# Performance work log

Measured on AMD Instinct MI355X. Metric: run time of the kernel, lower is better.

Reference implementation:

```python
import jax, jax.numpy as jnp
import numpy as np

GRID_SIZE = 5
SPLINE_ORDER = 3
NUM_EXPERTS = 8
TOP_K = 2
CAP_FACTOR = 1.25
TEMP = 1.0
GDHW = (4, 4, 4)


def make_grid(in_features):
    # efficient-KAN grid buffer: grid_range=[-1,1], extended by spline_order on each side
    h = 2.0 / GRID_SIZE
    g = jnp.arange(-SPLINE_ORDER, GRID_SIZE + SPLINE_ORDER + 1, dtype=jnp.float32) * h - 1.0
    return jnp.broadcast_to(g, (in_features, g.shape[0]))


def b_splines(x, grid):
    # x: (N, in) -> (N, in, GRID_SIZE + SPLINE_ORDER) Cox-de Boor bases
    x = x[:, :, None]
    bases = ((x >= grid[:, :-1]) & (x < grid[:, 1:])).astype(x.dtype)
    for k in range(1, SPLINE_ORDER + 1):
        left = (x - grid[:, : -(k + 1)]) / (grid[:, k:-1] - grid[:, : -(k + 1)])
        right = (grid[:, k + 1:] - x) / (grid[:, k + 1:] - grid[:, 1:-k])
        bases = left * bases[:, :, :-1] + right * bases[:, :, 1:]
    return bases


def kan_linear(x, base_w, spline_w, scaler, grid):
    base = jax.nn.silu(x) @ base_w.T
    bs = b_splines(x, grid)                                   # (N, in, coef)
    spline = jnp.einsum('nic,oic->no', bs, spline_w * scaler[:, :, None])
    return base + spline


def layernorm(x, w, b, eps=1e-5):
    mu = x.mean(-1, keepdims=True)
    var = x.var(-1, keepdims=True)
    return (x - mu) / jnp.sqrt(var + eps) * w + b


def setup_inputs() -> dict:
    key = jax.random.key(0)
    ks = jax.random.split(key, 12)
    Cf, hidden, E, nc = 256, 170, NUM_EXPERTS, 2
    coef = GRID_SIZE + SPLINE_ORDER
    def nrm(k, shape, scale):
        return jax.random.normal(k, shape, dtype=jnp.float32) * scale
    return {
        'fpn_feat': nrm(ks[0], (8, 254, 32, 32, 32), 1.0),
        'seg_logits': nrm(ks[1], (8, 2, 32, 32, 32), 1.0),
        'ln_r_w': jnp.ones((Cf,), jnp.float32),
        'ln_r_b': jnp.zeros((Cf,), jnp.float32),
        'ln_h_w': jnp.ones((Cf,), jnp.float32),
        'ln_h_b': jnp.zeros((Cf,), jnp.float32),
        'router_w': nrm(ks[2], (E, Cf), Cf ** -0.5),
        'router_b': jnp.zeros((E,), jnp.float32),
        'bw1': nrm(ks[3], (E, hidden, Cf), Cf ** -0.5),
        'sw1': nrm(ks[4], (E, hidden, Cf, coef), 0.1 * Cf ** -0.5),
        'sc1': nrm(ks[5], (E, hidden, Cf), Cf ** -0.5),
        'bw2': nrm(ks[6], (E, Cf, hidden), hidden ** -0.5),
        'sw2': nrm(ks[7], (E, Cf, hidden, coef), 0.1 * hidden ** -0.5),
        'sc2': nrm(ks[8], (E, Cf, hidden), hidden ** -0.5),
        'cls_bw': nrm(ks[9], (nc, Cf), Cf ** -0.5),
        'cls_sw': nrm(ks[10], (nc, Cf, coef), 0.1 * Cf ** -0.5),
        'cls_sc': nrm(ks[11], (nc, Cf), Cf ** -0.5),
        'grid_cf': make_grid(Cf),
        'grid_hid': make_grid(hidden),
    }


def reference(fpn_feat, seg_logits, ln_r_w, ln_r_b, ln_h_w, ln_h_b,
              router_w, router_b, bw1, sw1, sc1, bw2, sw2, sc2,
              cls_bw, cls_sw, cls_sc, grid_cf, grid_hid):
    fused = jnp.concatenate([fpn_feat, seg_logits], axis=1)   # (B, Cf, D, H, W)
    B, C, D, H, W = fused.shape
    gd, gh, gw = GDHW
    dp, hp, wp = D // gd, H // gh, W // gw
    # split into gd*gh*gw blocks per sample
    blk = fused.reshape(B, C, gd, dp, gh, hp, gw, wp)
    blk = blk.transpose(0, 2, 4, 6, 1, 3, 5, 7).reshape(-1, C, dp, hp, wp)
    vec = blk.mean(axis=(2, 3, 4))                            # (N, Cf) global avg pool

    N = vec.shape[0]
    E = NUM_EXPERTS
    x_norm = layernorm(vec, ln_r_w, ln_r_b)
    scores = (x_norm @ router_w.T + router_b) / TEMP          # (N, E)
    top_val, top_idx = jax.lax.top_k(scores, TOP_K)
    top_w = jax.nn.softmax(top_val, axis=-1)
    capacity = int(CAP_FACTOR * N * TOP_K / E) + 1

    onehot = top_idx[None] == jnp.arange(E)[:, None, None]    # (E, N, K)
    sel = onehot.any(-1)                                      # (E, N)
    pos = jnp.cumsum(sel.astype(jnp.int32), axis=1)           # rank among selected (1-based)
    keep = sel & (pos <= capacity)                            # capacity drop = first-come order
    w = (top_w[None] * onehot.astype(top_w.dtype)).sum(-1)    # (E, N) combine weights

    def expert(bw1e, sw1e, sc1e, bw2e, sw2e, sc2e):
        h = kan_linear(x_norm, bw1e, sw1e, sc1e, grid_cf)
        h = jax.nn.gelu(h, approximate=False)                 # torch nn.GELU default (erf)
        return kan_linear(h, bw2e, sw2e, sc2e, grid_hid)

    y_all = jax.vmap(expert)(bw1, sw1, sc1, bw2, sw2, sc2)    # (E, N, Cf)
    out = jnp.einsum('en,enc->nc', keep.astype(vec.dtype) * w, y_all)

    conf = scores.max(-1)                                     # (N,)
    logits_blk = kan_linear(layernorm(out, ln_h_w, ln_h_b), cls_bw, cls_sw, cls_sc, grid_cf)
    P = gd * gh * gw
    weight = jax.nn.softmax(conf.reshape(B, P), axis=-1)[:, :, None]
    logits = (logits_blk.reshape(B, P, -1) * weight).sum(1)   # (B, num_classes)
    return logits
```

## Files before the change

kernel.cpp:

```cpp
#include <hip/hip_runtime.h>
#include <math.h>

#define CF 256
#define HID 170
#define NE 8
#define NTOK 512
#define K1 2304
#define K2P 1536
#define CAPACITY 161

typedef __bf16 bf16x8 __attribute__((ext_vector_type(8)));
typedef unsigned short u16x8 __attribute__((ext_vector_type(8)));
typedef float f32x4 __attribute__((ext_vector_type(4)));

__device__ __forceinline__ float silu_f(float x) { return x / (1.0f + expf(-x)); }
__device__ __forceinline__ float gelu_f(float x) {
    return 0.5f * x * (1.0f + erff(x * 0.70710678118654752f));
}

__device__ __forceinline__ unsigned short f2bf(float f) {
    unsigned int u = __float_as_uint(f);
    u = u + 0x7fffu + ((u >> 16) & 1u);
    return (unsigned short)(u >> 16);
}

__device__ __forceinline__ void bspline8(float x, float bs[8]) {
    float b[11];
#pragma unroll
    for (int j = 0; j < 11; ++j) {
        float g0 = (float)(j - 3) * 0.4f - 1.0f;
        float g1 = (float)(j - 2) * 0.4f - 1.0f;
        b[j] = (x >= g0 && x < g1) ? 1.0f : 0.0f;
    }
#pragma unroll
    for (int k = 1; k <= 3; ++k) {
        float inv = 2.5f / (float)k;
#pragma unroll
        for (int j = 0; j < 10 - (k - 1); ++j) {
            float gj   = (float)(j - 3) * 0.4f - 1.0f;
            float gjk1 = (float)(j - 2 + k) * 0.4f - 1.0f;
            b[j] = (x - gj) * inv * b[j] + (gjk1 - x) * inv * b[j + 1];
        }
    }
#pragma unroll
    for (int c = 0; c < 8; ++c) bs[c] = b[c];
}

__global__ __launch_bounds__(256) void mega_front_kernel(const float* __restrict__ fpn,
                                                         const float* __restrict__ seg,
                                                         const float* __restrict__ bw1,
                                                         const float* __restrict__ sw1,
                                                         const float* __restrict__ sc1,
                                                         const float* __restrict__ bw2,
                                                         const float* __restrict__ sw2,
                                                         const float* __restrict__ sc2,
                                                         float* __restrict__ vec,
                                                         unsigned short* __restrict__ W1,
                                                         unsigned short* __restrict__ W2,
                                                         float* __restrict__ out) {
    int id = blockIdx.x, tid = threadIdx.x;
    if (id == 8192 && tid < 16) out[tid] = 0.0f;
    if (id < 8192) {
        int c = id & 255, bd = (id >> 8) & 3, b = id >> 10;
        const float* src = (c < 254) ? fpn + (size_t)(b * 254 + c) * 32768
                                     : seg + (size_t)(b * 2 + (c - 254)) * 32768;
        const float4* s4 = (const float4*)src + (size_t)bd * 8 * 256;
        float s = 0.0f;
#pragma unroll
        for (int it = 0; it < 8; ++it) {
            float4 v = s4[it * 256 + tid];
            s += v.x + v.y + v.z + v.w;
        }
        __shared__ float acc[16];
        if (tid < 16) acc[tid] = 0.0f;
        __syncthreads();
        int bh = tid >> 6, bw = (tid & 7) >> 1;
        atomicAdd(&acc[bh * 4 + bw], s);
        __syncthreads();
        if (tid < 16)
            vec[(size_t)(b * 64 + bd * 16 + tid) * CF + c] = acc[tid] * (1.0f / 512.0f);
    } else if (id < 8192 + NE * HID) {
        int r = id - 8192;
        int o = r % HID, e = r / HID, i = tid;
        size_t oi = (size_t)(e * HID + o) * CF + i;
        unsigned short* row = W1 + (size_t)(e * HID + o) * K1;
        row[i] = f2bf(bw1[oi]);
        float sc = sc1[oi];
        const float* sw = sw1 + oi * 8;
        u16x8 pk;
#pragma unroll
        for (int c = 0; c < 8; ++c) pk[c] = f2bf(sw[c] * sc);
        *(u16x8*)(row + CF + i * 8) = pk;
    } else {
        int r = id - (8192 + NE * HID);
        int o = r & 255, e = r >> 8, t = tid;
        unsigned short* row = W2 + (size_t)(e * CF + o) * K2P;
        if (t < HID) {
            size_t oi = (size_t)(e * CF + o) * HID + t;
            row[t] = f2bf(bw2[oi]);
            float sc = sc2[oi];
            const float* sw = sw2 + oi * 8;
            u16x8 pk;
#pragma unroll
            for (int c = 0; c < 8; ++c) pk[c] = f2bf(sw[c] * sc);
            *(u16x8*)(row + HID + t * 8) = pk;
        } else if (t < HID + 6) {
            row[HID * 9 + (t - HID)] = 0;
        }
    }
}

__global__ __launch_bounds__(256) void ln_score_a1_kernel(const float* __restrict__ vec,
                                                          const float* __restrict__ lnw,
                                                          const float* __restrict__ lnb,
                                                          const float* __restrict__ rw,
                                                          const float* __restrict__ rb,
                                                          float* __restrict__ scores,
                                                          unsigned short* __restrict__ A1,
                                                          unsigned short* __restrict__ A2) {
    int n = blockIdx.x, i = threadIdx.x;
    if (i < 48) {
        int e = i / 6, j = i - e * 6;
        A2[((size_t)e * NTOK + n) * K2P + HID * 9 + j] = 0;
    }
    float v = vec[(size_t)n * CF + i];
    float s1 = v, s2 = v * v;
#pragma unroll
    for (int off = 32; off > 0; off >>= 1) {
        s1 += __shfl_xor(s1, off);
        s2 += __shfl_xor(s2, off);
    }
    __shared__ float rs1[4], rs2[4];
    int lane = i & 63, wid = i >> 6;
    if (lane == 0) { rs1[wid] = s1; rs2[wid] = s2; }
    __syncthreads();
    float tot1 = rs1[0] + rs1[1] + rs1[2] + rs1[3];
    float tot2 = rs2[0] + rs2[1] + rs2[2] + rs2[3];
    float mu = tot1 * (1.0f / CF);
    float var = tot2 * (1.0f / CF) - mu * mu;
    float rsd = rsqrtf(var + 1e-5f);
    float xv = (v - mu) * rsd * lnw[i] + lnb[i];
    unsigned short* r = A1 + (size_t)n * K1;
    r[i] = f2bf(silu_f(xv));
    float bs[8]; bspline8(xv, bs);
    u16x8 pk;
#pragma unroll
    for (int c = 0; c < 8; ++c) pk[c] = f2bf(bs[c]);
    *(u16x8*)(r + CF + i * 8) = pk;
    float p[NE];
#pragma unroll
    for (int e = 0; e < NE; ++e) p[e] = xv * rw[e * CF + i];
#pragma unroll
    for (int off = 32; off > 0; off >>= 1)
#pragma unroll
        for (int e = 0; e < NE; ++e) p[e] += __shfl_xor(p[e], off);
    __shared__ float pacc[4][NE];
    if (lane == 0)
#pragma unroll
        for (int e = 0; e < NE; ++e) pacc[wid][e] = p[e];
    __syncthreads();
    if (i < NE)
        scores[n * NE + i] = pacc[0][i] + pacc[1][i] + pacc[2][i] + pacc[3][i] + rb[i];
}

template <int MODE, int NTX, int TPE>
__global__ __launch_bounds__(256) void gemm_mfma_kernel(
        const unsigned short* __restrict__ Ag, const unsigned short* __restrict__ Bg,
        float* __restrict__ C, unsigned short* __restrict__ A2,
        const float* __restrict__ scores, float* __restrict__ cw, float* __restrict__ conf,
        int N, int K, long sA, long sB, long sC, int ldc) {
    __shared__ alignas(16) unsigned char smem[65536];
    int tid = threadIdx.x;
    int lane = tid & 63, w = tid >> 6;

    if (MODE == 1 && blockIdx.x >= NE * TPE) {
        int* ti0 = (int*)smem;
        int* ti1 = ti0 + NTOK;
        float* tw0 = (float*)(ti1 + NTOK);
        float* tw1 = tw0 + NTOK;
#pragma unroll
        for (int half = 0; half < 2; ++half) {
            int t = half * 256 + tid;
            float m1 = -1e30f, m2 = -1e30f; int i1 = 0, i2 = 0;
#pragma unroll
            for (int e = 0; e < NE; ++e) {
                float sc = scores[t * NE + e];
                if (sc > m1) { m2 = m1; i2 = i1; m1 = sc; i1 = e; }
                else if (sc > m2) { m2 = sc; i2 = e; }
            }
            conf[t] = m1;
            float ew = expf(m2 - m1);
            ti0[t] = i1; ti1[t] = i2;
            tw0[t] = 1.0f / (1.0f + ew); tw1[t] = ew / (1.0f + ew);
        }
        __syncthreads();
#pragma unroll
        for (int e2 = 0; e2 < 2; ++e2) {
            int e = w * 2 + e2;
            int cnt = 0;
#pragma unroll
            for (int c = 0; c < NTOK / 64; ++c) {
                int t = c * 64 + lane;
                int h0 = (ti0[t] == e), h1 = (ti1[t] == e);
                int sel = h0 | h1;
                unsigned long long mask = __ballot(sel);
                int pos = cnt + (int)__popcll(mask & ((1ull << lane) - 1ull));
                float wv = 0.f;
                if (sel && pos < CAPACITY) wv = h0 ? tw0[t] : tw1[t];
                cw[e * NTOK + t] = wv;
                cnt += (int)__popcll(mask);
            }
        }
        return;
    }

    unsigned char* AsB = smem;
    unsigned char* BsB = smem + 32768;

    int bid = blockIdx.x;
    int e = bid & 7, t = bid >> 3;
    int m0 = (t / NTX) * 64, n0 = (t % NTX) * 64;
    const unsigned short* A = Ag + (size_t)e * sA;
    const unsigned short* B = Bg + (size_t)e * sB;
    int wr = w >> 1, wc = w & 1;
    int fr = lane & 15, fg = lane >> 4;

    int r0 = tid >> 5, ch = tid & 31;
    int d0 = r0 * 512 + ((ch * 16) ^ ((r0 & 7) << 4));
    const unsigned short* aP = A + (size_t)(m0 + r0) * K + ch * 8;
    const unsigned short* bP = B + (size_t)(n0 + r0) * K + ch * 8;
    bool bOk[8];
#pragma unroll
    for (int q = 0; q < 8; ++q) bOk[q] = (n0 + r0 + q * 8) < N;
    const u16x8 zero8 = {0, 0, 0, 0, 0, 0, 0, 0};

    f32x4 acc[2][2];
#pragma unroll
    for (int i = 0; i < 2; ++i)
#pragma unroll
        for (int j = 0; j < 2; ++j)
#pragma unroll
            for (int r = 0; r < 4; ++r) acc[i][j][r] = 0.f;

    const int steps = K >> 8;
    u16x8 ra[8], rb[8];
#pragma unroll
    for (int q = 0; q < 8; ++q) {
        ra[q] = *(const u16x8*)(aP + (size_t)q * 8 * K);
        rb[q] = bOk[q] ? *(const u16x8*)(bP + (size_t)q * 8 * K) : zero8;
    }

    for (int s = 0; s < steps; ++s) {
        __syncthreads();
#pragma unroll
        for (int q = 0; q < 8; ++q) {
            *(u16x8*)(AsB + d0 + q * 4096) = ra[q];
            *(u16x8*)(BsB + d0 + q * 4096) = rb[q];
        }
        __syncthreads();
        if (s + 1 < steps) {
            int k0 = (s + 1) << 8;
#pragma unroll
            for (int q = 0; q < 8; ++q) {
                ra[q] = *(const u16x8*)(aP + (size_t)q * 8 * K + k0);
                rb[q] = bOk[q] ? *(const u16x8*)(bP + (size_t)q * 8 * K + k0) : zero8;
            }
        }
#pragma unroll
        for (int ks = 0; ks < 8; ++ks) {
            int kb = ks * 64 + fg * 16;
            u16x8 af[2], bf[2];
#pragma unroll
            for (int mf = 0; mf < 2; ++mf) {
                int row = wr * 32 + mf * 16 + fr;
                af[mf] = *(const u16x8*)(AsB + row * 512 + (kb ^ ((row & 7) << 4)));
            }
#pragma unroll
            for (int nf = 0; nf < 2; ++nf) {
                int row = wc * 32 + nf * 16 + fr;
                bf[nf] = *(const u16x8*)(BsB + row * 512 + (kb ^ ((row & 7) << 4)));
            }
#pragma unroll
            for (int mf = 0; mf < 2; ++mf)
#pragma unroll
                for (int nf = 0; nf < 2; ++nf)
                    acc[mf][nf] = __builtin_amdgcn_mfma_f32_16x16x32_bf16(
                        __builtin_bit_cast(bf16x8, af[mf]),
                        __builtin_bit_cast(bf16x8, bf[nf]), acc[mf][nf], 0, 0, 0);
        }
    }

    if (MODE == 1) {
#pragma unroll
        for (int mf = 0; mf < 2; ++mf)
#pragma unroll
            for (int nf = 0; nf < 2; ++nf)
#pragma unroll
                for (int r = 0; r < 4; ++r) {
                    int row = m0 + wr * 32 + mf * 16 + fg * 4 + r;
                    int col = n0 + wc * 32 + nf * 16 + fr;
                    if (col < N) {
                        float g = gelu_f(acc[mf][nf][r]);
                        unsigned short* rr = A2 + ((size_t)e * NTOK + row) * K2P;
                        rr[col] = f2bf(silu_f(g));
                        float bs[8]; bspline8(g, bs);
                        u16x8 pk;
#pragma unroll
                        for (int c = 0; c < 8; ++c) pk[c] = f2bf(bs[c]);
                        *(u16x8*)(rr + HID + col * 8) = pk;
                    }
                }
    } else {
        float* Ce = C + (size_t)e * sC;
#pragma unroll
        for (int mf = 0; mf < 2; ++mf)
#pragma unroll
            for (int nf = 0; nf < 2; ++nf)
#pragma unroll
                for (int r = 0; r < 4; ++r) {
                    int row = m0 + wr * 32 + mf * 16 + fg * 4 + r;
                    int col = n0 + wc * 32 + nf * 16 + fr;
                    if (col < N) Ce[(size_t)row * ldc + col] = acc[mf][nf][r];
                }
    }
}

__global__ __launch_bounds__(256) void combcls_kernel(const float* __restrict__ y,
                                                      const float* __restrict__ cw,
                                                      const float* __restrict__ conf,
                                                      const float* __restrict__ lnw,
                                                      const float* __restrict__ lnb,
                                                      const float* __restrict__ cbw,
                                                      const float* __restrict__ csw,
                                                      const float* __restrict__ csc,
                                                      float* __restrict__ out) {
    int n = blockIdx.x, i = threadIdx.x;
    float v = 0.f;
#pragma unroll
    for (int e = 0; e < NE; ++e)
        v += cw[e * NTOK + n] * y[((size_t)(e * NTOK + n)) * CF + i];
    float s1 = v, s2 = v * v;
#pragma unroll
    for (int off = 32; off > 0; off >>= 1) {
        s1 += __shfl_xor(s1, off);
        s2 += __shfl_xor(s2, off);
    }
    __shared__ float rA[4], rB[4], rP0[4], rP1[4];
    int lane = i & 63, wid = i >> 6;
    if (lane == 0) { rA[wid] = s1; rB[wid] = s2; }
    __syncthreads();
    float tot1 = rA[0] + rA[1] + rA[2] + rA[3];
    float tot2 = rB[0] + rB[1] + rB[2] + rB[3];
    float mu = tot1 * (1.0f / CF);
    float var = tot2 * (1.0f / CF) - mu * mu;
    float rs = rsqrtf(var + 1e-5f);
    float xh = (v - mu) * rs * lnw[i] + lnb[i];
    float si = silu_f(xh);
    float bs[8]; bspline8(xh, bs);
    float p0 = si * cbw[i], p1 = si * cbw[CF + i];
    float sp0 = 0.f, sp1 = 0.f;
#pragma unroll
    for (int c = 0; c < 8; ++c) {
        sp0 += bs[c] * csw[(size_t)i * 8 + c];
        sp1 += bs[c] * csw[(size_t)(CF + i) * 8 + c];
    }
    p0 += sp0 * csc[i];
    p1 += sp1 * csc[CF + i];
#pragma unroll
    for (int off = 32; off > 0; off >>= 1) {
        p0 += __shfl_xor(p0, off);
        p1 += __shfl_xor(p1, off);
    }
    if (lane == 0) { rP0[wid] = p0; rP1[wid] = p1; }
    __syncthreads();
    if (i < 64) {
        int b = n >> 6;
        float cf = conf[b * 64 + i];
        float mx = cf;
#pragma unroll
        for (int off = 32; off > 0; off >>= 1) mx = fmaxf(mx, __shfl_xor(mx, off));
        float ev = expf(cf - mx);
        float sum = ev;
#pragma unroll
        for (int off = 32; off > 0; off >>= 1) sum += __shfl_xor(sum, off);
        if (i == 0) {
            float wself = expf(conf[n] - mx) / sum;
            float l0 = rP0[0] + rP0[1] + rP0[2] + rP0[3];
            float l1 = rP1[0] + rP1[1] + rP1[2] + rP1[3];
            atomicAdd(&out[b * 2 + 0], wself * l0);
            atomicAdd(&out[b * 2 + 1], wself * l1);
        }
    }
}

extern "C" void kernel_launch(void* const* d_in, const int* in_sizes, int n_in,
                              void* d_out, int out_size, void* d_ws, size_t ws_size,
                              hipStream_t stream) {
    const float* fpn      = (const float*)d_in[0];
    const float* seg      = (const float*)d_in[1];
    const float* ln_r_w   = (const float*)d_in[2];
    const float* ln_r_b   = (const float*)d_in[3];
    const float* ln_h_w   = (const float*)d_in[4];
    const float* ln_h_b   = (const float*)d_in[5];
    const float* router_w = (const float*)d_in[6];
    const float* router_b = (const float*)d_in[7];
    const float* bw1      = (const float*)d_in[8];
    const float* sw1      = (const float*)d_in[9];
    const float* sc1      = (const float*)d_in[10];
    const float* bw2      = (const float*)d_in[11];
    const float* sw2      = (const float*)d_in[12];
    const float* sc2      = (const float*)d_in[13];
    const float* cls_bw   = (const float*)d_in[14];
    const float* cls_sw   = (const float*)d_in[15];
    const float* cls_sc   = (const float*)d_in[16];
    float* out = (float*)d_out;

    float* ws = (float*)d_ws;
    float* vec    = ws;
    float* scores = vec + 131072;
    float* cw     = scores + 4096;
    float* conf   = cw + 4096;
    float* yall   = conf + 512;
    unsigned short* A1b = (unsigned short*)(yall + 1048576);
    unsigned short* W1b = A1b + (size_t)NTOK * K1;
    unsigned short* A2b = W1b + (size_t)NE * HID * K1;
    unsigned short* W2b = A2b + (size_t)NE * NTOK * K2P;

    mega_front_kernel<<<dim3(8192 + NE * HID + 2048), dim3(256), 0, stream>>>(
        fpn, seg, bw1, sw1, sc1, bw2, sw2, sc2, vec, W1b, W2b, out);
    ln_score_a1_kernel<<<dim3(NTOK), dim3(256), 0, stream>>>(vec, ln_r_w, ln_r_b, router_w,
                                                             router_b, scores, A1b, A2b);
    gemm_mfma_kernel<1, 3, 24><<<dim3(NE * 24 + 1), dim3(256), 0, stream>>>(
        A1b, W1b, nullptr, A2b, scores, cw, conf, HID, K1, 0L, (long)HID * K1, 0L, 0);
    gemm_mfma_kernel<0, 4, 32><<<dim3(NE * 32), dim3(256), 0, stream>>>(
        A2b, W2b, yall, nullptr, nullptr, nullptr, nullptr, CF, K2P, (long)NTOK * K2P,
        (long)CF * K2P, (long)NTOK * CF, CF);
    combcls_kernel<<<dim3(NTOK), dim3(256), 0, stream>>>(yall, cw, conf, ln_h_w, ln_h_b,
                                                         cls_bw, cls_sw, cls_sc, out);
}
```

Before: 111.3 us.

## Load MFMA operands directly from global memory, dropping LDS staging

Each wave now loads its A and B fragments straight from global memory into registers, one 32-wide k-slice at a time, with a one-step register prefetch. The shared-memory tile staging, XOR swizzle and the two barriers per k-step are gone, and the 64KB LDS buffer shrinks to the small routing arrays. This cuts LDS traffic and synchronisation and should raise occupancy, but neighbouring waves now fetch the same rows again from global memory or cache. Each lane also issues narrow 16-byte strided reads, and there is much less latency hiding per iteration.

Result: slower. 143.4 us (+28.9%).

```diff
diff --git a/kernel.cpp b/kernel.cpp
--- a/kernel.cpp
+++ b/kernel.cpp
@@ -169,15 +169,12 @@
         float* __restrict__ C, unsigned short* __restrict__ A2,
         const float* __restrict__ scores, float* __restrict__ cw, float* __restrict__ conf,
         int N, int K, long sA, long sB, long sC, int ldc) {
-    __shared__ alignas(16) unsigned char smem[65536];
+    __shared__ int   ti0[NTOK], ti1[NTOK];
+    __shared__ float tw0[NTOK], tw1[NTOK];
     int tid = threadIdx.x;
     int lane = tid & 63, w = tid >> 6;
 
     if (MODE == 1 && blockIdx.x >= NE * TPE) {
-        int* ti0 = (int*)smem;
-        int* ti1 = ti0 + NTOK;
-        float* tw0 = (float*)(ti1 + NTOK);
-        float* tw1 = tw0 + NTOK;
 #pragma unroll
         for (int half = 0; half < 2; ++half) {
             int t = half * 256 + tid;
@@ -214,9 +211,6 @@
         return;
     }
 
-    unsigned char* AsB = smem;
-    unsigned char* BsB = smem + 32768;
-
     int bid = blockIdx.x;
     int e = bid & 7, t = bid >> 3;
     int m0 = (t / NTX) * 64, n0 = (t % NTX) * 64;
@@ -225,14 +219,14 @@
     int wr = w >> 1, wc = w & 1;
     int fr = lane & 15, fg = lane >> 4;
 
-    int r0 = tid >> 5, ch = tid & 31;
-    int d0 = r0 * 512 + ((ch * 16) ^ ((r0 & 7) << 4));
-    const unsigned short* aP = A + (size_t)(m0 + r0) * K + ch * 8;
-    const unsigned short* bP = B + (size_t)(n0 + r0) * K + ch * 8;
-    bool bOk[8];
-#pragma unroll
-    for (int q = 0; q < 8; ++q) bOk[q] = (n0 + r0 + q * 8) < N;
-    const u16x8 zero8 = {0, 0, 0, 0, 0, 0, 0, 0};
+    int ar0 = m0 + wr * 32 + fr, ar1 = ar0 + 16;
+    int bc0 = n0 + wc * 32 + fr, bc1 = bc0 + 16;
+    int bb0 = bc0 < N ? bc0 : N - 1;
+    int bb1 = bc1 < N ? bc1 : N - 1;
+    const unsigned short* pa0 = A + (size_t)ar0 * K + fg * 8;
+    const unsigned short* pa1 = A + (size_t)ar1 * K + fg * 8;
+    const unsigned short* pb0 = B + (size_t)bb0 * K + fg * 8;
+    const unsigned short* pb1 = B + (size_t)bb1 * K + fg * 8;
 
     f32x4 acc[2][2];
 #pragma unroll
@@ -242,52 +236,30 @@
 #pragma unroll
             for (int r = 0; r < 4; ++r) acc[i][j][r] = 0.f;
 
-    const int steps = K >> 8;
-    u16x8 ra[8], rb[8];
-#pragma unroll
-    for (int q = 0; q < 8; ++q) {
-        ra[q] = *(const u16x8*)(aP + (size_t)q * 8 * K);
-        rb[q] = bOk[q] ? *(const u16x8*)(bP + (size_t)q * 8 * K) : zero8;
-    }
-
+    const int steps = K >> 5;
+    u16x8 a0 = *(const u16x8*)pa0;
+    u16x8 a1 = *(const u16x8*)pa1;
+    u16x8 b0 = *(const u16x8*)pb0;
+    u16x8 b1 = *(const u16x8*)pb1;
+#pragma unroll 4
     for (int s = 0; s < steps; ++s) {
-        __syncthreads();
-#pragma unroll
-        for (int q = 0; q < 8; ++q) {
-            *(u16x8*)(AsB + d0 + q * 4096) = ra[q];
-            *(u16x8*)(BsB + d0 + q * 4096) = rb[q];
-        }
-        __syncthreads();
+        u16x8 na0 = a0, na1 = a1, nb0 = b0, nb1 = b1;
         if (s + 1 < steps) {
-            int k0 = (s + 1) << 8;
-#pragma unroll
-            for (int q = 0; q < 8; ++q) {
-                ra[q] = *(const u16x8*)(aP + (size_t)q * 8 * K + k0);
-                rb[q] = bOk[q] ? *(const u16x8*)(bP + (size_t)q * 8 * K + k0) : zero8;
-            }
-        }
-#pragma unroll
-        for (int ks = 0; ks < 8; ++ks) {
-            int kb = ks * 64 + fg * 16;
-            u16x8 af[2], bf[2];
-#pragma unroll
-            for (int mf = 0; mf < 2; ++mf) {
-                int row = wr * 32 + mf * 16 + fr;
-                af[mf] = *(const u16x8*)(AsB + row * 512 + (kb ^ ((row & 7) << 4)));
-            }
-#pragma unroll
-            for (int nf = 0; nf < 2; ++nf) {
-                int row = wc * 32 + nf * 16 + fr;
-                bf[nf] = *(const u16x8*)(BsB + row * 512 + (kb ^ ((row & 7) << 4)));
-            }
-#pragma unroll
-            for (int mf = 0; mf < 2; ++mf)
-#pragma unroll
-                for (int nf = 0; nf < 2; ++nf)
-                    acc[mf][nf] = __builtin_amdgcn_mfma_f32_16x16x32_bf16(
-                        __builtin_bit_cast(bf16x8, af[mf]),
-                        __builtin_bit_cast(bf16x8, bf[nf]), acc[mf][nf], 0, 0, 0);
-        }
+            int k0 = (s + 1) << 5;
+            na0 = *(const u16x8*)(pa0 + k0);
+            na1 = *(const u16x8*)(pa1 + k0);
+            nb0 = *(const u16x8*)(pb0 + k0);
+            nb1 = *(const u16x8*)(pb1 + k0);
+        }
+        acc[0][0] = __builtin_amdgcn_mfma_f32_16x16x32_bf16(
+            __builtin_bit_cast(bf16x8, a0), __builtin_bit_cast(bf16x8, b0), acc[0][0], 0, 0, 0);
+        acc[0][1] = __builtin_amdgcn_mfma_f32_16x16x32_bf16(
+            __builtin_bit_cast(bf16x8, a0), __builtin_bit_cast(bf16x8, b1), acc[0][1], 0, 0, 0);
+        acc[1][0] = __builtin_amdgcn_mfma_f32_16x16x32_bf16(
+            __builtin_bit_cast(bf16x8, a1), __builtin_bit_cast(bf16x8, b0), acc[1][0], 0, 0, 0);
+        acc[1][1] = __builtin_amdgcn_mfma_f32_16x16x32_bf16(
+            __builtin_bit_cast(bf16x8, a1), __builtin_bit_cast(bf16x8, b1), acc[1][1], 0, 0, 0);
+        a0 = na0; a1 = na1; b0 = nb0; b1 = nb1;
     }
 
     if (MODE == 1) {
```

## Split GEMM K-loop across two warp groups with 512-thread blocks

Applied to the files above, without the earlier changes.

Doubles the GEMM block size to 512 threads and has the two halves of the warps each process half of every 256-wide K tile, then reduces the partial accumulators through shared memory. The global-to-LDS loads are spread over twice as many threads, so each thread holds fewer staging registers. The aim is more waves per CU to hide latency on a grid that has few blocks (193 and 256). The cost is an extra shared-memory reduction and sync at the end, plus higher register pressure under the 512 launch bound.

Result: no change. 109.8 us, median of 2 (-1.4%).

```diff
diff --git a/kernel.cpp b/kernel.cpp
--- a/kernel.cpp
+++ b/kernel.cpp
@@ -164,7 +164,7 @@
 }
 
 template <int MODE, int NTX, int TPE>
-__global__ __launch_bounds__(256) void gemm_mfma_kernel(
+__global__ __launch_bounds__(512) void gemm_mfma_kernel(
         const unsigned short* __restrict__ Ag, const unsigned short* __restrict__ Bg,
         float* __restrict__ C, unsigned short* __restrict__ A2,
         const float* __restrict__ scores, float* __restrict__ cw, float* __restrict__ conf,
@@ -178,9 +178,8 @@
         int* ti1 = ti0 + NTOK;
         float* tw0 = (float*)(ti1 + NTOK);
         float* tw1 = tw0 + NTOK;
-#pragma unroll
-        for (int half = 0; half < 2; ++half) {
-            int t = half * 256 + tid;
+        {
+            int t = tid;
             float m1 = -1e30f, m2 = -1e30f; int i1 = 0, i2 = 0;
 #pragma unroll
             for (int e = 0; e < NE; ++e) {
@@ -194,21 +193,23 @@
             tw0[t] = 1.0f / (1.0f + ew); tw1[t] = ew / (1.0f + ew);
         }
         __syncthreads();
-#pragma unroll
-        for (int e2 = 0; e2 < 2; ++e2) {
-            int e = w * 2 + e2;
-            int cnt = 0;
-#pragma unroll
-            for (int c = 0; c < NTOK / 64; ++c) {
-                int t = c * 64 + lane;
-                int h0 = (ti0[t] == e), h1 = (ti1[t] == e);
-                int sel = h0 | h1;
-                unsigned long long mask = __ballot(sel);
-                int pos = cnt + (int)__popcll(mask & ((1ull << lane) - 1ull));
-                float wv = 0.f;
-                if (sel && pos < CAPACITY) wv = h0 ? tw0[t] : tw1[t];
-                cw[e * NTOK + t] = wv;
-                cnt += (int)__popcll(mask);
+        if (w < 4) {
+#pragma unroll
+            for (int e2 = 0; e2 < 2; ++e2) {
+                int e = w * 2 + e2;
+                int cnt = 0;
+#pragma unroll
+                for (int c = 0; c < NTOK / 64; ++c) {
+                    int t = c * 64 + lane;
+                    int h0 = (ti0[t] == e), h1 = (ti1[t] == e);
+                    int sel = h0 | h1;
+                    unsigned long long mask = __ballot(sel);
+                    int pos = cnt + (int)__popcll(mask & ((1ull << lane) - 1ull));
+                    float wv = 0.f;
+                    if (sel && pos < CAPACITY) wv = h0 ? tw0[t] : tw1[t];
+                    cw[e * NTOK + t] = wv;
+                    cnt += (int)__popcll(mask);
+                }
             }
         }
         return;
@@ -222,16 +223,17 @@
     int m0 = (t / NTX) * 64, n0 = (t % NTX) * 64;
     const unsigned short* A = Ag + (size_t)e * sA;
     const unsigned short* B = Bg + (size_t)e * sB;
-    int wr = w >> 1, wc = w & 1;
+    int wrc = w & 3, kh = w >> 2;
+    int wr = wrc >> 1, wc = wrc & 1;
     int fr = lane & 15, fg = lane >> 4;
 
     int r0 = tid >> 5, ch = tid & 31;
     int d0 = r0 * 512 + ((ch * 16) ^ ((r0 & 7) << 4));
     const unsigned short* aP = A + (size_t)(m0 + r0) * K + ch * 8;
     const unsigned short* bP = B + (size_t)(n0 + r0) * K + ch * 8;
-    bool bOk[8];
-#pragma unroll
-    for (int q = 0; q < 8; ++q) bOk[q] = (n0 + r0 + q * 8) < N;
+    bool bOk[4];
+#pragma unroll
+    for (int q = 0; q < 4; ++q) bOk[q] = (n0 + r0 + q * 16) < N;
     const u16x8 zero8 = {0, 0, 0, 0, 0, 0, 0, 0};
 
     f32x4 acc[2][2];
@@ -243,32 +245,32 @@
             for (int r = 0; r < 4; ++r) acc[i][j][r] = 0.f;
 
     const int steps = K >> 8;
-    u16x8 ra[8], rb[8];
-#pragma unroll
-    for (int q = 0; q < 8; ++q) {
-        ra[q] = *(const u16x8*)(aP + (size_t)q * 8 * K);
-        rb[q] = bOk[q] ? *(const u16x8*)(bP + (size_t)q * 8 * K) : zero8;
+    u16x8 ra[4], rb[4];
+#pragma unroll
+    for (int q = 0; q < 4; ++q) {
+        ra[q] = *(const u16x8*)(aP + (size_t)q * 16 * K);
+        rb[q] = bOk[q] ? *(const u16x8*)(bP + (size_t)q * 16 * K) : zero8;
     }
 
     for (int s = 0; s < steps; ++s) {
         __syncthreads();
 #pragma unroll
-        for (int q = 0; q < 8; ++q) {
-            *(u16x8*)(AsB + d0 + q * 4096) = ra[q];
-            *(u16x8*)(BsB + d0 + q * 4096) = rb[q];
+        for (int q = 0; q < 4; ++q) {
+            *(u16x8*)(AsB + d0 + q * 8192) = ra[q];
+            *(u16x8*)(BsB + d0 + q * 8192) = rb[q];
         }
         __syncthreads();
         if (s + 1 < steps) {
             int k0 = (s + 1) << 8;
 #pragma unroll
-            for (int q = 0; q < 8; ++q) {
-                ra[q] = *(const u16x8*)(aP + (size_t)q * 8 * K + k0);
-                rb[q] = bOk[q] ? *(const u16x8*)(bP + (size_t)q * 8 * K + k0) : zero8;
+            for (int q = 0; q < 4; ++q) {
+                ra[q] = *(const u16x8*)(aP + (size_t)q * 16 * K + k0);
+                rb[q] = bOk[q] ? *(const u16x8*)(bP + (size_t)q * 16 * K + k0) : zero8;
             }
         }
 #pragma unroll
-        for (int ks = 0; ks < 8; ++ks) {
-            int kb = ks * 64 + fg * 16;
+        for (int ks = 0; ks < 4; ++ks) {
+            int kb = ((kh << 2) + ks) * 64 + fg * 16;
             u16x8 af[2], bf[2];
 #pragma unroll
             for (int mf = 0; mf < 2; ++mf) {
@@ -289,6 +291,27 @@
                         __builtin_bit_cast(bf16x8, bf[nf]), acc[mf][nf], 0, 0, 0);
         }
     }
+
+    __syncthreads();
+    float* xch = (float*)smem;
+    if (kh == 1) {
+#pragma unroll
+        for (int mf = 0; mf < 2; ++mf)
+#pragma unroll
+            for (int nf = 0; nf < 2; ++nf)
+#pragma unroll
+                for (int r = 0; r < 4; ++r)
+                    xch[(wrc * 64 + lane) * 16 + (mf * 2 + nf) * 4 + r] = acc[mf][nf][r];
+    }
+    __syncthreads();
+    if (kh == 1) return;
+#pragma unroll
+    for (int mf = 0; mf < 2; ++mf)
+#pragma unroll
+        for (int nf = 0; nf < 2; ++nf)
+#pragma unroll
+            for (int r = 0; r < 4; ++r)
+                acc[mf][nf][r] += xch[(wrc * 64 + lane) * 16 + (mf * 2 + nf) * 4 + r];
 
     if (MODE == 1) {
 #pragma unroll
@@ -430,9 +453,9 @@
         fpn, seg, bw1, sw1, sc1, bw2, sw2, sc2, vec, W1b, W2b, out);
     ln_score_a1_kernel<<<dim3(NTOK), dim3(256), 0, stream>>>(vec, ln_r_w, ln_r_b, router_w,
                                                              router_b, scores, A1b, A2b);
-    gemm_mfma_kernel<1, 3, 24><<<dim3(NE * 24 + 1), dim3(256), 0, stream>>>(
+    gemm_mfma_kernel<1, 3, 24><<<dim3(NE * 24 + 1), dim3(512), 0, stream>>>(
         A1b, W1b, nullptr, A2b, scores, cw, conf, HID, K1, 0L, (long)HID * K1, 0L, 0);
-    gemm_mfma_kernel<0, 4, 32><<<dim3(NE * 32), dim3(256), 0, stream>>>(
+    gemm_mfma_kernel<0, 4, 32><<<dim3(NE * 32), dim3(512), 0, stream>>>(
         A2b, W2b, yall, nullptr, nullptr, nullptr, nullptr, CF, K2P, (long)NTOK * K2P,
         (long)CF * K2P, (long)NTOK * CF, CF);
     combcls_kernel<<<dim3(NTOK), dim3(256), 0, stream>>>(yall, cw, conf, ln_h_w, ln_h_b,
```
